# Optimization experiments

Measured on AMD Instinct MI355X. Metric: run time of the kernel, lower is better.

## Reference

```python
import jax, jax.numpy as jnp
import numpy as np

B, S, D = 4, 4096, 256


def setup_inputs() -> dict:
    key = jax.random.key(0)
    ks = jax.random.split(key, 7)
    s = 1.0 / np.sqrt(D)
    return {
        "x": jax.random.normal(ks[0], (B, S, D), dtype=jnp.float32),
        "Wq": jax.random.uniform(ks[1], (D, D), jnp.float32, -s, s),
        "bq": jax.random.uniform(ks[2], (D,), jnp.float32, -s, s),
        "Wk": jax.random.uniform(ks[3], (D, D), jnp.float32, -s, s),
        "bk": jax.random.uniform(ks[4], (D,), jnp.float32, -s, s),
        "Wv": jax.random.uniform(ks[5], (D, D), jnp.float32, -s, s),
        "bv": jax.random.uniform(ks[6], (D,), jnp.float32, -s, s),
    }


def reference(x, Wq, bq, Wk, bk, Wv, bv):
    # nn.Linear: y = x @ W.T + b
    Q = jnp.einsum("bsd,ed->bse", x, Wq) + bq
    K = jnp.einsum("bsd,ed->bse", x, Wk) + bk
    V = jnp.einsum("bsd,ed->bse", x, Wv) + bv
    dk = Q.shape[-1]
    scores = jnp.einsum("bqd,bkd->bqk", Q, K) / jnp.sqrt(jnp.float32(dk))
    # NOTE: original applies softmax over dim=1 (the query axis), not -1.
    attn = jax.nn.softmax(scores, axis=1)
    out = jnp.einsum("bqk,bkd->bqd", attn, V)
    return out
```

## Files before the change

kernel.cpp:

```cpp
#include <hip/hip_runtime.h>

typedef short bf16x8 __attribute__((ext_vector_type(8)));
typedef float f32x4 __attribute__((ext_vector_type(4)));
typedef unsigned short u16;

#define S_LEN 4096
#define D_DIM 256
#define NROW  16384

__device__ __forceinline__ u16 f2bf(float f) {
    union { float f; unsigned u; } v; v.f = f;
    unsigned r = v.u + 0x7FFFu + ((v.u >> 16) & 1u);
    return (u16)(r >> 16);
}

__device__ __forceinline__ size_t fr_qk(int t, int kk) {
    return (size_t)t * 4096 + kk * 512;
}
__device__ __forceinline__ size_t fr_v(int p, int dt, int kk2) {
    return (size_t)p * 16384 + (dt * 2 + kk2) * 512;
}

__device__ __forceinline__ void gll16(const u16* g, u16* l) {
    __builtin_amdgcn_global_load_lds(
        (const __attribute__((address_space(1))) unsigned int*)g,
        (__attribute__((address_space(3))) unsigned int*)l, 16, 0, 0);
}

#define WAITV8 asm volatile("s_waitcnt vmcnt(8)" ::: "memory")
#define WAITV0 asm volatile("s_waitcnt vmcnt(0)" ::: "memory")
#define MEMFENCE asm volatile("" ::: "memory")

__global__ __launch_bounds__(256) void wconv(
    const float* __restrict__ Wq, const float* __restrict__ Wk,
    const float* __restrict__ Wv, u16* __restrict__ Wf)
{
    int i = blockIdx.x * 256 + threadIdx.x;
    int m = i >> 13;
    int idx = i & 8191;
    int ocol = idx >> 5;
    int d0 = (idx & 31) * 8;
    const float* s = (m == 0 ? Wq : (m == 1 ? Wk : Wv)) + ocol * 256 + d0;
    float4 v0 = *reinterpret_cast<const float4*>(s);
    float4 v1 = *reinterpret_cast<const float4*>(s + 4);
    union { ushort4 h[2]; int4 q; } t;
    t.h[0] = make_ushort4(f2bf(v0.x), f2bf(v0.y), f2bf(v0.z), f2bf(v0.w));
    t.h[1] = make_ushort4(f2bf(v1.x), f2bf(v1.y), f2bf(v1.z), f2bf(v1.w));
    size_t off = (size_t)m * 65536 + fr_qk(ocol >> 4, d0 >> 5)
               + ((d0 >> 3) & 3) * 128 + (ocol & 15) * 8;
    *reinterpret_cast<int4*>(Wf + off) = t.q;
}

__global__ __launch_bounds__(256) void qkv_proj(
    const float* __restrict__ x, const u16* __restrict__ Wf,
    const float* __restrict__ bq, const float* __restrict__ bk,
    const float* __restrict__ bv,
    u16* __restrict__ Qf, u16* __restrict__ Kf, u16* __restrict__ Vf)
{
    __shared__ u16 xs[32][264];
    const int tid = threadIdx.x;
    const int r0 = blockIdx.x * 32;

    #pragma unroll
    for (int i = 0; i < 8; ++i) {
        int c = i * 256 + tid;
        int row = c >> 6, c4 = c & 63;
        float4 v = reinterpret_cast<const float4*>(x + (size_t)(r0 + row) * D_DIM)[c4];
        *reinterpret_cast<ushort4*>(&xs[row][c4 * 4]) =
            make_ushort4(f2bf(v.x), f2bf(v.y), f2bf(v.z), f2bf(v.w));
    }
    __syncthreads();

    const int w = tid >> 6, l = tid & 63, lr = l & 15, lg = l >> 4;
    const int c0 = w * 64;

    bf16x8 a[2][8];
    #pragma unroll
    for (int qs = 0; qs < 2; ++qs)
        #pragma unroll
        for (int kk = 0; kk < 8; ++kk)
            a[qs][kk] = *reinterpret_cast<const bf16x8*>(&xs[qs * 16 + lr][kk * 32 + lg * 8]);

    const float* Bs[3] = {bq, bk, bv};

    #pragma unroll
    for (int m = 0; m < 3; ++m) {
        const u16* Wm = Wf + (size_t)m * 65536;
        f32x4 acc[2][4] = {};
        #pragma unroll
        for (int kk = 0; kk < 8; ++kk) {
            #pragma unroll
            for (int cf = 0; cf < 4; ++cf) {
                bf16x8 wfr = *reinterpret_cast<const bf16x8*>(
                    Wm + fr_qk(w * 4 + cf, kk) + l * 8);
                acc[0][cf] = __builtin_amdgcn_mfma_f32_16x16x32_bf16(a[0][kk], wfr, acc[0][cf], 0, 0, 0);
                acc[1][cf] = __builtin_amdgcn_mfma_f32_16x16x32_bf16(a[1][kk], wfr, acc[1][cf], 0, 0, 0);
            }
        }
        if (m < 2) {
            u16* outp = (m == 0) ? Qf : Kf;
            int t = r0 >> 4;
            #pragma unroll
            for (int qs = 0; qs < 2; ++qs) {
                #pragma unroll
                for (int cf = 0; cf < 4; ++cf) {
                    int col = c0 + cf * 16 + lr;
                    float bias = Bs[m][col];
                    size_t base = fr_qk(t + qs, col >> 5) + ((col >> 3) & 3) * 128 + (col & 7);
                    #pragma unroll
                    for (int r = 0; r < 4; ++r)
                        outp[base + (lg * 4 + r) * 8] = f2bf(acc[qs][cf][r] + bias);
                }
            }
        } else {
            int p  = (r0 >> 12) * 64 + ((r0 & 4095) >> 6);
            int kb = r0 & 63;
            #pragma unroll
            for (int qs = 0; qs < 2; ++qs) {
                #pragma unroll
                for (int cf = 0; cf < 4; ++cf) {
                    int d = c0 + cf * 16 + lr;
                    float bias = bv[d];
                    #pragma unroll
                    for (int r = 0; r < 4; ++r) {
                        int key = kb + qs * 16 + lg * 4 + r;
                        size_t off = fr_v(p, d >> 4, key >> 5)
                                   + ((key >> 3) & 3) * 128 + (d & 15) * 8 + (key & 7);
                        Vf[off] = f2bf(acc[qs][cf][r] + bias);
                    }
                }
            }
        }
    }
}

__global__ __launch_bounds__(256, 2) void col_denom(
    const u16* __restrict__ Qf, const u16* __restrict__ Kf, float* __restrict__ Zp)
{
    __shared__ __align__(16) u16 Qls[2][8192];
    const int tid = threadIdx.x, blk = blockIdx.x;
    const int xcd = blk & 7, sub = blk >> 3;
    const int b  = xcd >> 1;
    const int qq = ((xcd & 1) << 1) | (sub & 1);
    const int ktile = sub >> 1;
    const int w = tid >> 6, l = tid & 63, lr = l & 15, lg = l >> 4;
    const int k0 = ktile * 128;

    bf16x8 kreg[2][8];
    #pragma unroll
    for (int ks = 0; ks < 2; ++ks) {
        const int tk = b * 256 + (k0 >> 4) + w * 2 + ks;
        #pragma unroll
        for (int kk = 0; kk < 8; ++kk)
            kreg[ks][kk] = *reinterpret_cast<const bf16x8*>(Kf + fr_qk(tk, kk) + l * 8);
    }

    #define STAGE_Q(qt_, nb_) do { \
        const u16* g_ = Qf + ((size_t)(b * 256 + (qt_) * 2)) * 4096 + (w * 4) * 512 + l * 8; \
        u16* d_ = &Qls[nb_][(w * 4) * 512]; \
        _Pragma("unroll") \
        for (int f_ = 0; f_ < 4; ++f_) gll16(g_ + f_ * 512, d_ + f_ * 512); \
    } while (0)

    const int qt0 = qq * 32;
    STAGE_Q(qt0, 0);
    __syncthreads();

    float Z[2][4] = {};
    const float SC = 0.0625f;

    for (int it = 0; it < 32; ++it) {
        const int cur = it & 1;
        if (it < 31) STAGE_Q(qt0 + it + 1, cur ^ 1);

        f32x4 acc[2][2] = {};
        #pragma unroll
        for (int kk = 0; kk < 8; ++kk) {
            #pragma unroll
            for (int qf = 0; qf < 2; ++qf) {
                bf16x8 qfr = *reinterpret_cast<const bf16x8*>(
                    &Qls[cur][(qf * 8 + kk) * 512 + l * 8]);
                acc[0][qf] = __builtin_amdgcn_mfma_f32_16x16x32_bf16(kreg[0][kk], qfr, acc[0][qf], 0, 0, 0);
                acc[1][qf] = __builtin_amdgcn_mfma_f32_16x16x32_bf16(kreg[1][kk], qfr, acc[1][qf], 0, 0, 0);
            }
        }
        #pragma unroll
        for (int ks = 0; ks < 2; ++ks)
            #pragma unroll
            for (int qf = 0; qf < 2; ++qf)
                #pragma unroll
                for (int r = 0; r < 4; ++r)
                    Z[ks][r] += __expf(acc[ks][qf][r] * SC);
        __syncthreads();
    }

    #pragma unroll
    for (int ks = 0; ks < 2; ++ks) {
        #pragma unroll
        for (int r = 0; r < 4; ++r) {
            float z = Z[ks][r];
            z += __shfl_xor(z, 1);
            z += __shfl_xor(z, 2);
            z += __shfl_xor(z, 4);
            z += __shfl_xor(z, 8);
            if (lr == 0)
                Zp[qq * NROW + b * S_LEN + k0 + w * 32 + ks * 16 + lg * 4 + r] = z;
        }
    }
    #undef STAGE_Q
}

__global__ __launch_bounds__(256) void zlog(
    const float* __restrict__ Zp, float* __restrict__ LZ)
{
    int i = blockIdx.x * 256 + threadIdx.x;
    LZ[i] = logf(((Zp[i] + Zp[NROW + i]) + Zp[2 * NROW + i]) + Zp[3 * NROW + i]);
}

__global__ __launch_bounds__(512, 1) void attn_out(
    const u16* __restrict__ Qf, const u16* __restrict__ Kf, const u16* __restrict__ Vf,
    const float* __restrict__ LZ, float* __restrict__ out)
{
    __shared__ __align__(16) u16 Kls[4][8192];
    __shared__ __align__(16) u16 Vls[4][8192];
    __shared__ __align__(16) u16 ps[8][1280];

    const int tid = threadIdx.x, blk = blockIdx.x;
    const int xcd = blk & 7, sub = blk >> 3;
    const int b  = xcd >> 1;
    const int kq = ((xcd & 1) << 1) | (sub & 1);
    const int qtile = sub >> 1;
    const int w = tid >> 6, l = tid & 63, lr = l & 15, lg = l >> 4;
    const int q0 = qtile * 256 + w * 32;
    const int base_tk = b * 256;
    const int kt0 = kq * 32;

    bf16x8 qreg[2][8];
    #pragma unroll
    for (int qs = 0; qs < 2; ++qs) {
        const int tq = base_tk + ((q0 + qs * 16) >> 4);
        #pragma unroll
        for (int kk = 0; kk < 8; ++kk)
            qreg[qs][kk] = *reinterpret_cast<const bf16x8*>(Qf + fr_qk(tq, kk) + l * 8);
    }

    #define STAGE(kt_, nb_) do { \
        if (w < 4) { \
            const u16* g_ = Kf + ((size_t)(base_tk + (kt0 + (kt_)) * 2)) * 4096 + (w * 4) * 512 + l * 8; \
            u16* d_ = &Kls[nb_][(w * 4) * 512]; \
            _Pragma("unroll") \
            for (int f_ = 0; f_ < 4; ++f_) gll16(g_ + f_ * 512, d_ + f_ * 512); \
        } else { \
            const int kta_ = kt0 + (kt_); \
            const size_t vb_ = ((size_t)(b * 64 + (kta_ >> 1))) * 16384 + (kta_ & 1) * 512; \
            const int dt0_ = (w - 4) * 4; \
            _Pragma("unroll") \
            for (int f_ = 0; f_ < 4; ++f_) \
                gll16(Vf + vb_ + (size_t)(dt0_ + f_) * 1024 + l * 8, &Vls[nb_][(dt0_ + f_) * 512]); \
        } \
    } while (0)

    #define BODY(kt_) do { \
        const int cur_ = (kt_) & 3; \
        const int ktabs_ = kt0 + (kt_); \
        _Pragma("unroll") \
        for (int cf = 0; cf < 2; ++cf) { \
            float Lv = LZ[b * S_LEN + ktabs_ * 32 + cf * 16 + lr]; \
            f32x4 sacc[2] = {}; \
            __builtin_amdgcn_s_setprio(1); \
            _Pragma("unroll") \
            for (int kk = 0; kk < 8; ++kk) { \
                bf16x8 kfr = *reinterpret_cast<const bf16x8*>( \
                    &Kls[cur_][(cf * 8 + kk) * 512 + l * 8]); \
                sacc[0] = __builtin_amdgcn_mfma_f32_16x16x32_bf16(qreg[0][kk], kfr, sacc[0], 0, 0, 0); \
                sacc[1] = __builtin_amdgcn_mfma_f32_16x16x32_bf16(qreg[1][kk], kfr, sacc[1], 0, 0, 0); \
            } \
            __builtin_amdgcn_s_setprio(0); \
            _Pragma("unroll") \
            for (int qs = 0; qs < 2; ++qs) \
                _Pragma("unroll") \
                for (int r = 0; r < 4; ++r) { \
                    float p = __expf(fmaf(sacc[qs][r], SC, -Lv)); \
                    ps[w][(qs * 16 + lg * 4 + r) * 40 + cf * 16 + lr] = f2bf(p); \
                } \
        } \
        { \
            bf16x8 af0 = *reinterpret_cast<const bf16x8*>(&ps[w][lr * 40 + lg * 8]); \
            bf16x8 af1 = *reinterpret_cast<const bf16x8*>(&ps[w][(16 + lr) * 40 + lg * 8]); \
            __builtin_amdgcn_s_setprio(1); \
            _Pragma("unroll") \
            for (int dt = 0; dt < 16; ++dt) { \
                bf16x8 vfr = *reinterpret_cast<const bf16x8*>(&Vls[cur_][dt * 512 + l * 8]); \
                oacc[0][dt] = __builtin_amdgcn_mfma_f32_16x16x32_bf16(af0, vfr, oacc[0][dt], 0, 0, 0); \
                oacc[1][dt] = __builtin_amdgcn_mfma_f32_16x16x32_bf16(af1, vfr, oacc[1][dt], 0, 0, 0); \
            } \
            __builtin_amdgcn_s_setprio(0); \
        } \
    } while (0)

    f32x4 oacc[2][16] = {};
    const float SC = 0.0625f;

    STAGE(0, 0);
    STAGE(1, 1);
    STAGE(2, 2);
    WAITV8;
    __builtin_amdgcn_s_barrier();
    MEMFENCE;

    #pragma unroll 1
    for (int kt = 0; kt < 29; ++kt) {
        STAGE(kt + 3, (kt + 3) & 3);
        BODY(kt);
        WAITV8;
        __builtin_amdgcn_s_barrier();
        MEMFENCE;
    }
    #pragma unroll 1
    for (int kt = 29; kt < 32; ++kt) {
        BODY(kt);
        if (kt < 31) {
            WAITV0;
            __builtin_amdgcn_s_barrier();
            MEMFENCE;
        }
    }

    #pragma unroll
    for (int qs = 0; qs < 2; ++qs) {
        #pragma unroll
        for (int dt = 0; dt < 16; ++dt) {
            #pragma unroll
            for (int r = 0; r < 4; ++r) {
                int row = q0 + qs * 16 + lg * 4 + r;
                unsafeAtomicAdd(&out[((size_t)(b * S_LEN + row)) * D_DIM + dt * 16 + lr],
                                oacc[qs][dt][r]);
            }
        }
    }
    #undef STAGE
    #undef BODY
}

extern "C" void kernel_launch(void* const* d_in, const int* in_sizes, int n_in,
                              void* d_out, int out_size, void* d_ws, size_t ws_size,
                              hipStream_t stream) {
    const float* x  = (const float*)d_in[0];
    const float* Wq = (const float*)d_in[1];
    const float* bq = (const float*)d_in[2];
    const float* Wk = (const float*)d_in[3];
    const float* bk = (const float*)d_in[4];
    const float* Wv = (const float*)d_in[5];
    const float* bv = (const float*)d_in[6];
    float* out = (float*)d_out;

    u16* Qf = (u16*)d_ws;
    u16* Kf = Qf + (size_t)NROW * D_DIM;
    u16* Vf = Kf + (size_t)NROW * D_DIM;
    u16* Wf = Vf + (size_t)NROW * D_DIM;
    float* Zp = (float*)(Wf + 196608);
    float* LZ = Zp + 4 * NROW;

    hipMemsetAsync(out, 0, (size_t)NROW * D_DIM * sizeof(float), stream);

    wconv<<<96, 256, 0, stream>>>(Wq, Wk, Wv, Wf);
    qkv_proj<<<NROW / 32, 256, 0, stream>>>(x, Wf, bq, bk, bv, Qf, Kf, Vf);
    col_denom<<<512, 256, 0, stream>>>(Qf, Kf, Zp);
    zlog<<<NROW / 256, 256, 0, stream>>>(Zp, LZ);
    attn_out<<<256, 512, 0, stream>>>(Qf, Kf, Vf, LZ, out);
}
```

Baseline: 187.7 us.

## Software-pipeline QK and PV stages with double-buffered P and LDS-staged LZ

Restructures the attention-output main loop so each iteration computes QK scores for tile kt while running the PV matmul for tile kt-1. The softmax numerators are written to a double-buffered per-wave P tile, so the MFMA chains are no longer serialized behind the exp step. The K ring drops to 3 buffers with a prefetch distance of 2, while V keeps 4 buffers because it is consumed one step later. The log-normalizers for the block's key range are preloaded into LDS once instead of being read from global memory per tile. This trades shallower K prefetch and more live registers (sacc[2][2] plus oacc) for better MFMA/exp overlap, and risks register pressure or spilling.

```diff
diff --git a/kernel.cpp b/kernel.cpp
--- a/kernel.cpp
+++ b/kernel.cpp
@@ -27,8 +27,9 @@
         (__attribute__((address_space(3))) unsigned int*)l, 16, 0, 0);
 }
 
-#define WAITV8 asm volatile("s_waitcnt vmcnt(8)" ::: "memory")
+#define WAITV4 asm volatile("s_waitcnt vmcnt(4)" ::: "memory")
 #define WAITV0 asm volatile("s_waitcnt vmcnt(0)" ::: "memory")
+#define WAITLGKM0 asm volatile("s_waitcnt lgkmcnt(0)" ::: "memory")
 #define MEMFENCE asm volatile("" ::: "memory")
 
 __global__ __launch_bounds__(256) void wconv(
@@ -221,9 +222,10 @@
     const u16* __restrict__ Qf, const u16* __restrict__ Kf, const u16* __restrict__ Vf,
     const float* __restrict__ LZ, float* __restrict__ out)
 {
-    __shared__ __align__(16) u16 Kls[4][8192];
+    __shared__ __align__(16) u16 Kls[3][8192];
     __shared__ __align__(16) u16 Vls[4][8192];
-    __shared__ __align__(16) u16 ps[8][1280];
+    __shared__ __align__(16) u16 ps[8][2][1280];
+    __shared__ __align__(16) float lzs[1024];
 
     const int tid = threadIdx.x, blk = blockIdx.x;
     const int xcd = blk & 7, sub = blk >> 3;
@@ -244,10 +246,10 @@
             qreg[qs][kk] = *reinterpret_cast<const bf16x8*>(Qf + fr_qk(tq, kk) + l * 8);
     }
 
-    #define STAGE(kt_, nb_) do { \
+    #define STAGE(kt_) do { \
         if (w < 4) { \
             const u16* g_ = Kf + ((size_t)(base_tk + (kt0 + (kt_)) * 2)) * 4096 + (w * 4) * 512 + l * 8; \
-            u16* d_ = &Kls[nb_][(w * 4) * 512]; \
+            u16* d_ = &Kls[(kt_) % 3][(w * 4) * 512]; \
             _Pragma("unroll") \
             for (int f_ = 0; f_ < 4; ++f_) gll16(g_ + f_ * 512, d_ + f_ * 512); \
         } else { \
@@ -256,74 +258,96 @@
             const int dt0_ = (w - 4) * 4; \
             _Pragma("unroll") \
             for (int f_ = 0; f_ < 4; ++f_) \
-                gll16(Vf + vb_ + (size_t)(dt0_ + f_) * 1024 + l * 8, &Vls[nb_][(dt0_ + f_) * 512]); \
+                gll16(Vf + vb_ + (size_t)(dt0_ + f_) * 1024 + l * 8, &Vls[(kt_) % 4][(dt0_ + f_) * 512]); \
         } \
     } while (0)
 
-    #define BODY(kt_) do { \
-        const int cur_ = (kt_) & 3; \
-        const int ktabs_ = kt0 + (kt_); \
+    #define QK(kt_) do { \
+        const u16* kb_ = &Kls[(kt_) % 3][0]; \
+        __builtin_amdgcn_s_setprio(1); \
+        _Pragma("unroll") \
+        for (int kk = 0; kk < 8; ++kk) { \
+            bf16x8 k0_ = *reinterpret_cast<const bf16x8*>(kb_ + kk * 512 + l * 8); \
+            bf16x8 k1_ = *reinterpret_cast<const bf16x8*>(kb_ + (8 + kk) * 512 + l * 8); \
+            sacc[0][0] = __builtin_amdgcn_mfma_f32_16x16x32_bf16(qreg[0][kk], k0_, sacc[0][0], 0, 0, 0); \
+            sacc[0][1] = __builtin_amdgcn_mfma_f32_16x16x32_bf16(qreg[1][kk], k0_, sacc[0][1], 0, 0, 0); \
+            sacc[1][0] = __builtin_amdgcn_mfma_f32_16x16x32_bf16(qreg[0][kk], k1_, sacc[1][0], 0, 0, 0); \
+            sacc[1][1] = __builtin_amdgcn_mfma_f32_16x16x32_bf16(qreg[1][kk], k1_, sacc[1][1], 0, 0, 0); \
+        } \
+        __builtin_amdgcn_s_setprio(0); \
+    } while (0)
+
+    #define PV(j_) do { \
+        const u16* vb_ = &Vls[(j_) % 4][0]; \
+        const u16* pb_ = &ps[w][(j_) & 1][0]; \
+        bf16x8 af0_ = *reinterpret_cast<const bf16x8*>(pb_ + lr * 40 + lg * 8); \
+        bf16x8 af1_ = *reinterpret_cast<const bf16x8*>(pb_ + (16 + lr) * 40 + lg * 8); \
+        __builtin_amdgcn_s_setprio(1); \
+        _Pragma("unroll") \
+        for (int dt = 0; dt < 16; ++dt) { \
+            bf16x8 vf_ = *reinterpret_cast<const bf16x8*>(vb_ + dt * 512 + l * 8); \
+            oacc[0][dt] = __builtin_amdgcn_mfma_f32_16x16x32_bf16(af0_, vf_, oacc[0][dt], 0, 0, 0); \
+            oacc[1][dt] = __builtin_amdgcn_mfma_f32_16x16x32_bf16(af1_, vf_, oacc[1][dt], 0, 0, 0); \
+        } \
+        __builtin_amdgcn_s_setprio(0); \
+    } while (0)
+
+    #define SM(kt_) do { \
+        u16* pw_ = &ps[w][(kt_) & 1][0]; \
         _Pragma("unroll") \
         for (int cf = 0; cf < 2; ++cf) { \
-            float Lv = LZ[b * S_LEN + ktabs_ * 32 + cf * 16 + lr]; \
-            f32x4 sacc[2] = {}; \
-            __builtin_amdgcn_s_setprio(1); \
-            _Pragma("unroll") \
-            for (int kk = 0; kk < 8; ++kk) { \
-                bf16x8 kfr = *reinterpret_cast<const bf16x8*>( \
-                    &Kls[cur_][(cf * 8 + kk) * 512 + l * 8]); \
-                sacc[0] = __builtin_amdgcn_mfma_f32_16x16x32_bf16(qreg[0][kk], kfr, sacc[0], 0, 0, 0); \
-                sacc[1] = __builtin_amdgcn_mfma_f32_16x16x32_bf16(qreg[1][kk], kfr, sacc[1], 0, 0, 0); \
-            } \
-            __builtin_amdgcn_s_setprio(0); \
+            float Lv_ = lzs[(kt_) * 32 + cf * 16 + lr]; \
             _Pragma("unroll") \
             for (int qs = 0; qs < 2; ++qs) \
                 _Pragma("unroll") \
                 for (int r = 0; r < 4; ++r) { \
-                    float p = __expf(fmaf(sacc[qs][r], SC, -Lv)); \
-                    ps[w][(qs * 16 + lg * 4 + r) * 40 + cf * 16 + lr] = f2bf(p); \
+                    float p_ = __expf(fmaf(sacc[cf][qs][r], SC, -Lv_)); \
+                    pw_[(qs * 16 + lg * 4 + r) * 40 + cf * 16 + lr] = f2bf(p_); \
                 } \
         } \
-        { \
-            bf16x8 af0 = *reinterpret_cast<const bf16x8*>(&ps[w][lr * 40 + lg * 8]); \
-            bf16x8 af1 = *reinterpret_cast<const bf16x8*>(&ps[w][(16 + lr) * 40 + lg * 8]); \
-            __builtin_amdgcn_s_setprio(1); \
-            _Pragma("unroll") \
-            for (int dt = 0; dt < 16; ++dt) { \
-                bf16x8 vfr = *reinterpret_cast<const bf16x8*>(&Vls[cur_][dt * 512 + l * 8]); \
-                oacc[0][dt] = __builtin_amdgcn_mfma_f32_16x16x32_bf16(af0, vfr, oacc[0][dt], 0, 0, 0); \
-                oacc[1][dt] = __builtin_amdgcn_mfma_f32_16x16x32_bf16(af1, vfr, oacc[1][dt], 0, 0, 0); \
-            } \
-            __builtin_amdgcn_s_setprio(0); \
-        } \
     } while (0)
 
     f32x4 oacc[2][16] = {};
     const float SC = 0.0625f;
 
-    STAGE(0, 0);
-    STAGE(1, 1);
-    STAGE(2, 2);
-    WAITV8;
+    f32x4 lzv;
+    if (tid < 256)
+        lzv = *reinterpret_cast<const f32x4*>(LZ + b * S_LEN + kt0 * 32 + tid * 4);
+    STAGE(0);
+    STAGE(1);
+    if (tid < 256)
+        *reinterpret_cast<f32x4*>(&lzs[tid * 4]) = lzv;
+    WAITLGKM0;
+    WAITV4;
     __builtin_amdgcn_s_barrier();
     MEMFENCE;
 
     #pragma unroll 1
-    for (int kt = 0; kt < 29; ++kt) {
-        STAGE(kt + 3, (kt + 3) & 3);
-        BODY(kt);
-        WAITV8;
+    for (int kt = 0; kt < 30; ++kt) {
+        STAGE(kt + 2);
+        f32x4 sacc[2][2] = {};
+        QK(kt);
+        if (kt > 0) PV(kt - 1);
+        SM(kt);
+        WAITV4;
         __builtin_amdgcn_s_barrier();
         MEMFENCE;
     }
-    #pragma unroll 1
-    for (int kt = 29; kt < 32; ++kt) {
-        BODY(kt);
-        if (kt < 31) {
-            WAITV0;
-            __builtin_amdgcn_s_barrier();
-            MEMFENCE;
-        }
+    {
+        f32x4 sacc[2][2] = {};
+        QK(30);
+        PV(29);
+        SM(30);
+        WAITV0;
+        __builtin_amdgcn_s_barrier();
+        MEMFENCE;
+    }
+    {
+        f32x4 sacc[2][2] = {};
+        QK(31);
+        PV(30);
+        SM(31);
+        PV(31);
     }
 
     #pragma unroll
@@ -339,7 +363,9 @@
         }
     }
     #undef STAGE
-    #undef BODY
+    #undef QK
+    #undef PV
+    #undef SM
 }
 
 extern "C" void kernel_launch(void* const* d_in, const int* in_sizes, int n_in,
```

New measurement: 181.0 us. -3.6%, faster.
